# Kernel tuning notes

Measured on AMD Instinct MI355X. Metric: run time of the kernel, lower is better.

## Reference

```python
import jax, jax.numpy as jnp
import numpy as np

STD_MIN = 1e-05
MAX_VAL = 100.0

B, T, C = 16, 8192, 128


def setup_inputs() -> dict:
    key = jax.random.key(0)
    k1, k2 = jax.random.split(key)
    x = jax.random.normal(k1, (B, T, C), dtype=jnp.float32)
    # binary missing-value mask (1 = missing), stored as float per mask.float() in torch
    mask = jax.random.randint(k2, (B, T, C), 0, 2).astype(jnp.float32)
    return {"x": x, "mask": mask}


def reference(x, mask):
    # valid-count running along time: n_t = cumsum(1 - mask)
    nm = 1.0 - mask                      # [B,T,C], 1 where observed
    n = jnp.cumsum(nm, axis=1)
    n = jnp.where(n == 0, 1.0, n)        # avoid div-by-zero before first valid point
    # causal running mean (note: cumsum of x includes masked entries, as in original)
    mean = jax.lax.stop_gradient(jnp.cumsum(x, axis=1) / n)
    # causal running std over masked squared deviations
    std = jnp.sqrt(jnp.cumsum(((x - mean) * nm) ** 2, axis=1) / n)
    std = jnp.where(std > STD_MIN, std, 1.0)
    std = jax.lax.stop_gradient(std)
    return jnp.clip((x - mean) / std, -MAX_VAL, MAX_VAL)
```

## Files before the change

kernel.cpp:

```cpp
#include <hip/hip_runtime.h>
#include <math.h>
#include <stdint.h>

constexpr int B = 16;
constexpr int T = 8192;
constexpr int C = 128;
constexpr int CG = C / 4;
constexpr int TBK = 128;
constexpr int NCH = T / TBK;
constexpr int SUBS = 8;
constexpr int RPT = TBK / SUBS;
constexpr float STD_MIN = 1e-5f;
constexpr float MAX_VAL = 100.0f;

using f32x4 = __attribute__((ext_vector_type(4))) float;

__device__ inline f32x4 sel_neff(f32x4 n) {
    f32x4 r;
    #pragma unroll
    for (int j = 0; j < 4; ++j) r[j] = (n[j] == 0.0f) ? 1.0f : n[j];
    return r;
}
__device__ inline f32x4 rcp4(f32x4 a) {
    f32x4 r;
    #pragma unroll
    for (int j = 0; j < 4; ++j) r[j] = __builtin_amdgcn_rcpf(a[j]);
    return r;
}
__device__ inline f32x4 sqrt4(f32x4 a) {
    f32x4 r;
    #pragma unroll
    for (int j = 0; j < 4; ++j) r[j] = __builtin_amdgcn_sqrtf(a[j]);
    return r;
}
__device__ inline f32x4 decode_nib(unsigned nib) {
    f32x4 r;
    r[0] = (float)(nib & 1u);
    r[1] = (float)((nib >> 1) & 1u);
    r[2] = (float)((nib >> 2) & 1u);
    r[3] = (float)((nib >> 3) & 1u);
    return r;
}

__global__ __launch_bounds__(256) void k1_sums(
    const f32x4* __restrict__ x, const f32x4* __restrict__ mask,
    f32x4* __restrict__ aggx, f32x4* __restrict__ aggn,
    uint64_t* __restrict__ nmw)
{
    __shared__ f32x4 p0[SUBS][CG], p1[SUBS][CG];
    int tid = threadIdx.x, cg = tid & 31, sub = tid >> 5;
    int blk = blockIdx.x, b = blk >> 6, k = blk & (NCH - 1);
    size_t base = ((size_t)b * T + (size_t)k * TBK + (size_t)sub * RPT) * CG + cg;

    f32x4 sx = {0,0,0,0}, sn = {0,0,0,0};
    uint64_t w = 0;
    #pragma unroll
    for (int r = 0; r < RPT; ++r) {
        f32x4 xv = x[base + (size_t)r * CG];
        f32x4 mv = mask[base + (size_t)r * CG];
        f32x4 nm = 1.0f - mv;
        sx += xv; sn += nm;
        unsigned nib = (unsigned)nm[0] | ((unsigned)nm[1] << 1)
                     | ((unsigned)nm[2] << 2) | ((unsigned)nm[3] << 3);
        w |= (uint64_t)nib << (4 * r);
    }
    nmw[(size_t)blk * 256 + tid] = w;
    p0[sub][cg] = sx; p1[sub][cg] = sn;
    __syncthreads();
    if (sub == 0) {
        f32x4 tx = p0[0][cg], tn = p1[0][cg];
        #pragma unroll
        for (int s = 1; s < SUBS; ++s) { tx += p0[s][cg]; tn += p1[s][cg]; }
        aggx[(size_t)blk * CG + cg] = tx;
        aggn[(size_t)blk * CG + cg] = tn;
    }
}

__global__ __launch_bounds__(256) void k2_dev2(
    const f32x4* __restrict__ x,
    const f32x4* __restrict__ aggx, const f32x4* __restrict__ aggn,
    const uint64_t* __restrict__ nmw, f32x4* __restrict__ aggd)
{
    __shared__ f32x4 p0[SUBS][CG], p1[SUBS][CG];
    int tid = threadIdx.x, cg = tid & 31, sub = tid >> 5;
    int blk = blockIdx.x, b = blk >> 6, k = blk & (NCH - 1);
    size_t base = ((size_t)b * T + (size_t)k * TBK + (size_t)sub * RPT) * CG + cg;

    f32x4 pxp = {0,0,0,0}, pnp = {0,0,0,0};
    for (int j = sub; j < k; j += SUBS) {
        size_t o = ((size_t)(b * NCH + j)) * CG + cg;
        pxp += aggx[o]; pnp += aggn[o];
    }
    p0[sub][cg] = pxp; p1[sub][cg] = pnp;
    __syncthreads();
    f32x4 px = p0[0][cg], pn = p1[0][cg];
    #pragma unroll
    for (int s = 1; s < SUBS; ++s) { px += p0[s][cg]; pn += p1[s][cg]; }

    f32x4 xr[RPT];
    #pragma unroll
    for (int r = 0; r < RPT; ++r) xr[r] = x[base + (size_t)r * CG];
    uint64_t w = nmw[(size_t)blk * 256 + tid];

    f32x4 sx = {0,0,0,0}, sn = {0,0,0,0};
    #pragma unroll
    for (int r = 0; r < RPT; ++r) {
        sx += xr[r];
        sn += decode_nib((unsigned)(w >> (4 * r)) & 0xFu);
    }
    __syncthreads();
    p0[sub][cg] = sx; p1[sub][cg] = sn;
    __syncthreads();
    f32x4 offx = {0,0,0,0}, offn = {0,0,0,0};
    for (int s = 0; s < sub; ++s) { offx += p0[s][cg]; offn += p1[s][cg]; }

    f32x4 rx = px + offx, rn = pn + offn, sd = {0,0,0,0};
    #pragma unroll
    for (int r = 0; r < RPT; ++r) {
        f32x4 nm = decode_nib((unsigned)(w >> (4 * r)) & 0xFu);
        rx += xr[r]; rn += nm;
        f32x4 mean = rx * rcp4(sel_neff(rn));
        f32x4 d = (xr[r] - mean) * nm;
        sd += d * d;
    }
    __syncthreads();
    p0[sub][cg] = sd;
    __syncthreads();
    if (sub == 0) {
        f32x4 td = p0[0][cg];
        #pragma unroll
        for (int s = 1; s < SUBS; ++s) td += p0[s][cg];
        aggd[(size_t)blk * CG + cg] = td;
    }
}

__global__ __launch_bounds__(256) void k3_final(
    const f32x4* __restrict__ x,
    const f32x4* __restrict__ aggx, const f32x4* __restrict__ aggn,
    const f32x4* __restrict__ aggd, const uint64_t* __restrict__ nmw,
    f32x4* __restrict__ out)
{
    __shared__ f32x4 p0[SUBS][CG], p1[SUBS][CG], p2[SUBS][CG];
    int tid = threadIdx.x, cg = tid & 31, sub = tid >> 5;
    int blk = blockIdx.x, b = blk >> 6, k = blk & (NCH - 1);
    size_t base = ((size_t)b * T + (size_t)k * TBK + (size_t)sub * RPT) * CG + cg;

    f32x4 pxp = {0,0,0,0}, pnp = {0,0,0,0}, pdp = {0,0,0,0};
    for (int j = sub; j < k; j += SUBS) {
        size_t o = ((size_t)(b * NCH + j)) * CG + cg;
        pxp += aggx[o]; pnp += aggn[o]; pdp += aggd[o];
    }
    p0[sub][cg] = pxp; p1[sub][cg] = pnp; p2[sub][cg] = pdp;
    __syncthreads();
    f32x4 px = p0[0][cg], pn = p1[0][cg], pd = p2[0][cg];
    #pragma unroll
    for (int s = 1; s < SUBS; ++s) {
        px += p0[s][cg]; pn += p1[s][cg]; pd += p2[s][cg];
    }

    f32x4 xr[RPT];
    #pragma unroll
    for (int r = 0; r < RPT; ++r) xr[r] = x[base + (size_t)r * CG];
    uint64_t w = nmw[(size_t)blk * 256 + tid];

    f32x4 sx = {0,0,0,0}, sn = {0,0,0,0};
    #pragma unroll
    for (int r = 0; r < RPT; ++r) {
        sx += xr[r];
        sn += decode_nib((unsigned)(w >> (4 * r)) & 0xFu);
    }
    __syncthreads();
    p0[sub][cg] = sx; p1[sub][cg] = sn;
    __syncthreads();
    f32x4 offx = {0,0,0,0}, offn = {0,0,0,0};
    for (int s = 0; s < sub; ++s) { offx += p0[s][cg]; offn += p1[s][cg]; }
    f32x4 rx0 = px + offx, rn0 = pn + offn;

    f32x4 rx = rx0, rn = rn0, sd = {0,0,0,0};
    #pragma unroll
    for (int r = 0; r < RPT; ++r) {
        f32x4 nm = decode_nib((unsigned)(w >> (4 * r)) & 0xFu);
        rx += xr[r]; rn += nm;
        f32x4 mean = rx * rcp4(sel_neff(rn));
        f32x4 d = (xr[r] - mean) * nm;
        sd += d * d;
    }
    __syncthreads();
    p0[sub][cg] = sd;
    __syncthreads();
    f32x4 offd = {0,0,0,0};
    for (int s = 0; s < sub; ++s) offd += p0[s][cg];
    f32x4 rd = pd + offd;

    rx = rx0; rn = rn0;
    #pragma unroll
    for (int r = 0; r < RPT; ++r) {
        f32x4 nm = decode_nib((unsigned)(w >> (4 * r)) & 0xFu);
        rx += xr[r]; rn += nm;
        f32x4 inv = rcp4(sel_neff(rn));
        f32x4 mean = rx * inv;
        f32x4 d = (xr[r] - mean) * nm;
        rd += d * d;
        f32x4 s = sqrt4(rd * inv);
        f32x4 ov;
        #pragma unroll
        for (int j = 0; j < 4; ++j) {
            float invs = (s[j] > STD_MIN) ? __builtin_amdgcn_rcpf(s[j]) : 1.0f;
            float v = (xr[r][j] - mean[j]) * invs;
            ov[j] = fminf(fmaxf(v, -MAX_VAL), MAX_VAL);
        }
        __builtin_nontemporal_store(ov, &out[base + (size_t)r * CG]);
    }
}

extern "C" void kernel_launch(void* const* d_in, const int* in_sizes, int n_in,
                              void* d_out, int out_size, void* d_ws, size_t ws_size,
                              hipStream_t stream) {
    const f32x4* x    = (const f32x4*)d_in[0];
    const f32x4* mask = (const f32x4*)d_in[1];
    f32x4* out = (f32x4*)d_out;

    size_t agg_elems = (size_t)B * NCH * CG;
    f32x4* aggx = (f32x4*)d_ws;
    f32x4* aggn = aggx + agg_elems;
    f32x4* aggd = aggn + agg_elems;
    uint64_t* nmw = (uint64_t*)(aggd + agg_elems);

    int grid = B * NCH;

    k1_sums<<<grid, 256, 0, stream>>>(x, mask, aggx, aggn, nmw);
    k2_dev2<<<grid, 256, 0, stream>>>(x, aggx, aggn, nmw, aggd);
    k3_final<<<grid, 256, 0, stream>>>(x, aggx, aggn, aggd, nmw, out);
}
```

Baseline: 72.94 us.

## Persist per-subchunk partial sums to skip recomputation in later kernels

The first pass now writes each sub-chunk's x and valid-count partial sums to workspace, and the second pass writes its per-sub-chunk squared-deviation sums. The later kernels read those stored prefixes directly. This drops the in-block recomputation passes, several shared-memory syncs and the register arrays that held x, so x is streamed once per kernel. The costs are extra global workspace traffic (about 1/16 of x's size per stored partial array) and a larger workspace. The zero-count select is also replaced by max(n, 1), which gives the same result for non-negative counts.

```diff
diff --git a/kernel.cpp b/kernel.cpp
--- a/kernel.cpp
+++ b/kernel.cpp
@@ -15,10 +15,10 @@
 
 using f32x4 = __attribute__((ext_vector_type(4))) float;
 
-__device__ inline f32x4 sel_neff(f32x4 n) {
-    f32x4 r;
-    #pragma unroll
-    for (int j = 0; j < 4; ++j) r[j] = (n[j] == 0.0f) ? 1.0f : n[j];
+__device__ inline f32x4 max1(f32x4 n) {
+    f32x4 r;
+    #pragma unroll
+    for (int j = 0; j < 4; ++j) r[j] = fmaxf(n[j], 1.0f);
     return r;
 }
 __device__ inline f32x4 rcp4(f32x4 a) {
@@ -45,6 +45,7 @@
 __global__ __launch_bounds__(256) void k1_sums(
     const f32x4* __restrict__ x, const f32x4* __restrict__ mask,
     f32x4* __restrict__ aggx, f32x4* __restrict__ aggn,
+    f32x4* __restrict__ subx, f32x4* __restrict__ subn,
     uint64_t* __restrict__ nmw)
 {
     __shared__ f32x4 p0[SUBS][CG], p1[SUBS][CG];
@@ -65,6 +66,9 @@
         w |= (uint64_t)nib << (4 * r);
     }
     nmw[(size_t)blk * 256 + tid] = w;
+    size_t so = ((size_t)blk * SUBS + sub) * CG + cg;
+    subx[so] = sx;
+    subn[so] = sn;
     p0[sub][cg] = sx; p1[sub][cg] = sn;
     __syncthreads();
     if (sub == 0) {
@@ -79,7 +83,9 @@
 __global__ __launch_bounds__(256) void k2_dev2(
     const f32x4* __restrict__ x,
     const f32x4* __restrict__ aggx, const f32x4* __restrict__ aggn,
-    const uint64_t* __restrict__ nmw, f32x4* __restrict__ aggd)
+    const f32x4* __restrict__ subx, const f32x4* __restrict__ subn,
+    const uint64_t* __restrict__ nmw,
+    f32x4* __restrict__ aggd, f32x4* __restrict__ subd)
 {
     __shared__ f32x4 p0[SUBS][CG], p1[SUBS][CG];
     int tid = threadIdx.x, cg = tid & 31, sub = tid >> 5;
@@ -97,32 +103,25 @@
     #pragma unroll
     for (int s = 1; s < SUBS; ++s) { px += p0[s][cg]; pn += p1[s][cg]; }
 
-    f32x4 xr[RPT];
-    #pragma unroll
-    for (int r = 0; r < RPT; ++r) xr[r] = x[base + (size_t)r * CG];
+    f32x4 offx = {0,0,0,0}, offn = {0,0,0,0};
+    for (int s = 0; s < sub; ++s) {
+        size_t so = ((size_t)blk * SUBS + s) * CG + cg;
+        offx += subx[so]; offn += subn[so];
+    }
+    f32x4 rx = px + offx, rn = pn + offn;
     uint64_t w = nmw[(size_t)blk * 256 + tid];
 
-    f32x4 sx = {0,0,0,0}, sn = {0,0,0,0};
+    f32x4 sd = {0,0,0,0};
     #pragma unroll
     for (int r = 0; r < RPT; ++r) {
-        sx += xr[r];
-        sn += decode_nib((unsigned)(w >> (4 * r)) & 0xFu);
-    }
-    __syncthreads();
-    p0[sub][cg] = sx; p1[sub][cg] = sn;
-    __syncthreads();
-    f32x4 offx = {0,0,0,0}, offn = {0,0,0,0};
-    for (int s = 0; s < sub; ++s) { offx += p0[s][cg]; offn += p1[s][cg]; }
-
-    f32x4 rx = px + offx, rn = pn + offn, sd = {0,0,0,0};
-    #pragma unroll
-    for (int r = 0; r < RPT; ++r) {
+        f32x4 xv = x[base + (size_t)r * CG];
         f32x4 nm = decode_nib((unsigned)(w >> (4 * r)) & 0xFu);
-        rx += xr[r]; rn += nm;
-        f32x4 mean = rx * rcp4(sel_neff(rn));
-        f32x4 d = (xr[r] - mean) * nm;
+        rx += xv; rn += nm;
+        f32x4 mean = rx * rcp4(max1(rn));
+        f32x4 d = (xv - mean) * nm;
         sd += d * d;
     }
+    subd[((size_t)blk * SUBS + sub) * CG + cg] = sd;
     __syncthreads();
     p0[sub][cg] = sd;
     __syncthreads();
@@ -137,8 +136,10 @@
 __global__ __launch_bounds__(256) void k3_final(
     const f32x4* __restrict__ x,
     const f32x4* __restrict__ aggx, const f32x4* __restrict__ aggn,
-    const f32x4* __restrict__ aggd, const uint64_t* __restrict__ nmw,
-    f32x4* __restrict__ out)
+    const f32x4* __restrict__ aggd,
+    const f32x4* __restrict__ subx, const f32x4* __restrict__ subn,
+    const f32x4* __restrict__ subd,
+    const uint64_t* __restrict__ nmw, f32x4* __restrict__ out)
 {
     __shared__ f32x4 p0[SUBS][CG], p1[SUBS][CG], p2[SUBS][CG];
     int tid = threadIdx.x, cg = tid & 31, sub = tid >> 5;
@@ -158,55 +159,29 @@
         px += p0[s][cg]; pn += p1[s][cg]; pd += p2[s][cg];
     }
 
-    f32x4 xr[RPT];
-    #pragma unroll
-    for (int r = 0; r < RPT; ++r) xr[r] = x[base + (size_t)r * CG];
+    f32x4 offx = {0,0,0,0}, offn = {0,0,0,0}, offd = {0,0,0,0};
+    for (int s = 0; s < sub; ++s) {
+        size_t so = ((size_t)blk * SUBS + s) * CG + cg;
+        offx += subx[so]; offn += subn[so]; offd += subd[so];
+    }
+    f32x4 rx = px + offx, rn = pn + offn, rd = pd + offd;
     uint64_t w = nmw[(size_t)blk * 256 + tid];
 
-    f32x4 sx = {0,0,0,0}, sn = {0,0,0,0};
     #pragma unroll
     for (int r = 0; r < RPT; ++r) {
-        sx += xr[r];
-        sn += decode_nib((unsigned)(w >> (4 * r)) & 0xFu);
-    }
-    __syncthreads();
-    p0[sub][cg] = sx; p1[sub][cg] = sn;
-    __syncthreads();
-    f32x4 offx = {0,0,0,0}, offn = {0,0,0,0};
-    for (int s = 0; s < sub; ++s) { offx += p0[s][cg]; offn += p1[s][cg]; }
-    f32x4 rx0 = px + offx, rn0 = pn + offn;
-
-    f32x4 rx = rx0, rn = rn0, sd = {0,0,0,0};
-    #pragma unroll
-    for (int r = 0; r < RPT; ++r) {
+        f32x4 xv = x[base + (size_t)r * CG];
         f32x4 nm = decode_nib((unsigned)(w >> (4 * r)) & 0xFu);
-        rx += xr[r]; rn += nm;
-        f32x4 mean = rx * rcp4(sel_neff(rn));
-        f32x4 d = (xr[r] - mean) * nm;
-        sd += d * d;
-    }
-    __syncthreads();
-    p0[sub][cg] = sd;
-    __syncthreads();
-    f32x4 offd = {0,0,0,0};
-    for (int s = 0; s < sub; ++s) offd += p0[s][cg];
-    f32x4 rd = pd + offd;
-
-    rx = rx0; rn = rn0;
-    #pragma unroll
-    for (int r = 0; r < RPT; ++r) {
-        f32x4 nm = decode_nib((unsigned)(w >> (4 * r)) & 0xFu);
-        rx += xr[r]; rn += nm;
-        f32x4 inv = rcp4(sel_neff(rn));
+        rx += xv; rn += nm;
+        f32x4 inv = rcp4(max1(rn));
         f32x4 mean = rx * inv;
-        f32x4 d = (xr[r] - mean) * nm;
+        f32x4 d = (xv - mean) * nm;
         rd += d * d;
         f32x4 s = sqrt4(rd * inv);
         f32x4 ov;
         #pragma unroll
         for (int j = 0; j < 4; ++j) {
             float invs = (s[j] > STD_MIN) ? __builtin_amdgcn_rcpf(s[j]) : 1.0f;
-            float v = (xr[r][j] - mean[j]) * invs;
+            float v = (xv[j] - mean[j]) * invs;
             ov[j] = fminf(fmaxf(v, -MAX_VAL), MAX_VAL);
         }
         __builtin_nontemporal_store(ov, &out[base + (size_t)r * CG]);
@@ -221,14 +196,18 @@
     f32x4* out = (f32x4*)d_out;
 
     size_t agg_elems = (size_t)B * NCH * CG;
+    size_t sub_elems = (size_t)B * NCH * SUBS * CG;
     f32x4* aggx = (f32x4*)d_ws;
     f32x4* aggn = aggx + agg_elems;
     f32x4* aggd = aggn + agg_elems;
-    uint64_t* nmw = (uint64_t*)(aggd + agg_elems);
+    f32x4* subx = aggd + agg_elems;
+    f32x4* subn = subx + sub_elems;
+    f32x4* subd = subn + sub_elems;
+    uint64_t* nmw = (uint64_t*)(subd + sub_elems);
 
     int grid = B * NCH;
 
-    k1_sums<<<grid, 256, 0, stream>>>(x, mask, aggx, aggn, nmw);
-    k2_dev2<<<grid, 256, 0, stream>>>(x, aggx, aggn, nmw, aggd);
-    k3_final<<<grid, 256, 0, stream>>>(x, aggx, aggn, aggd, nmw, out);
-}
+    k1_sums<<<grid, 256, 0, stream>>>(x, mask, aggx, aggn, subx, subn, nmw);
+    k2_dev2<<<grid, 256, 0, stream>>>(x, aggx, aggn, subx, subn, nmw, aggd, subd);
+    k3_final<<<grid, 256, 0, stream>>>(x, aggx, aggn, aggd, subx, subn, subd, nmw, out);
+}
```

Measured after the change: 70.54 us (median of 2 runs). 3.3% less time.
